# Kernel optimization log

Hardware: AMD Instinct MI355X
Metric: run time of the kernel (lower is better)

## Reference

```python
import jax, jax.numpy as jnp
import numpy as np

CONV_NUM = 8
CONV_SIZE = 96
HIDDEN = 768  # = CONV_NUM * CONV_SIZE
MAX_LEN = 128


def get_entity(x, s, e):
    # x: [B, L, H]; mean of x[i, s[i]:max(e[i], s[i]+1)] per sample (ragged gather+mean)
    e = jnp.maximum(e, s + 1)
    pos = jnp.arange(x.shape[1])  # [L]
    mask = (pos[None, :] >= s[:, None]) & (pos[None, :] < e[:, None])  # [B, L]
    m = mask.astype(x.dtype)
    return jnp.einsum('blh,bl->bh', x, m) / jnp.sum(m, axis=1, keepdims=True)


def feature_abstract(head_ent, tail_ent, x, fc_W, fc_b):
    # head_ent/tail_ent: [B, HIDDEN] -> per-sample conv filters; x: [B, HIDDEN]
    B = x.shape[0]
    wh = head_ent.reshape(B * CONV_NUM, 1, 1, CONV_SIZE)
    wt = tail_ent.reshape(B * CONV_NUM, 1, 1, CONV_SIZE)
    lhs = x.reshape(1, B, 1, HIDDEN)  # NCHW, groups=B -> per-sample correlation
    h = jax.nn.relu(jax.lax.conv_general_dilated(lhs, wh, (1, 1), 'VALID', feature_group_count=B))
    t = jax.nn.relu(jax.lax.conv_general_dilated(lhs, wt, (1, 1), 'VALID', feature_group_count=B))
    # h,t: [1, B*CONV_NUM, 1, T] with T = HIDDEN - CONV_SIZE + 1
    ht = jnp.concatenate([h, t], axis=3).reshape(B * CONV_NUM, -1)  # [B*cn, 2T]
    ht = ht.reshape(B * CONV_NUM, -1, 2).mean(axis=-1)  # AvgPool1d(k=2, s=2) -> [B*cn, T]
    flat = ht.reshape(B, -1)  # [B, cn*T] (dropout is identity in eval)
    return flat @ fc_W.T + fc_b  # [B, HIDDEN]


def setup_inputs() -> dict:
    key = jax.random.key(0)
    ks = jax.random.split(key, 16)
    Bs, Bq, L, H = 400, 1200, MAX_LEN, HIDDEN

    def spans(k1, k2, B):
        s = jax.random.randint(k1, (B,), 0, 100)
        e = jnp.minimum(s + jax.random.randint(k2, (B,), 1, 20), L)
        return s.astype(jnp.int64), e.astype(jnp.int64)

    s_eh, s_eh_end = spans(ks[0], ks[1], Bs)
    s_et, s_et_end = spans(ks[2], ks[3], Bs)
    q_eh, q_eh_end = spans(ks[4], ks[5], Bq)
    q_et, q_et_end = spans(ks[6], ks[7], Bq)
    fc_in = (H - CONV_SIZE + 1) * CONV_NUM  # 5384
    return {
        'all_support': jax.random.normal(ks[8], (Bs, L, H), jnp.float32),
        'support_emb': jax.random.normal(ks[9], (Bs, H), jnp.float32),
        'all_query': jax.random.normal(ks[10], (Bq, L, H), jnp.float32),
        'query_emb': jax.random.normal(ks[11], (Bq, H), jnp.float32),
        'fc_W': jax.random.normal(ks[12], (H, fc_in), jnp.float32) / np.sqrt(fc_in),
        'fc_b': jnp.zeros((H,), jnp.float32),
        's_eh': s_eh, 's_eh_end': s_eh_end, 's_et': s_et, 's_et_end': s_et_end,
        'q_eh': q_eh, 'q_eh_end': q_eh_end, 'q_et': q_et, 'q_et_end': q_et_end,
        'N': 10, 'K': 5, 'total_Q': 150,
    }


def reference(all_support, support_emb, all_query, query_emb, fc_W, fc_b,
              s_eh, s_eh_end, s_et, s_et_end, q_eh, q_eh_end, q_et, q_et_end,
              N, K, total_Q):
    sh = get_entity(all_support, s_eh, s_eh_end)
    st = get_entity(all_support, s_et, s_et_end)
    qh = get_entity(all_query, q_eh, q_eh_end)
    qt = get_entity(all_query, q_et, q_et_end)

    sup = feature_abstract(sh, st, support_emb, fc_W, fc_b).reshape(-1, N, K, HIDDEN)
    qry = feature_abstract(qh, qt, query_emb, fc_W, fc_b).reshape(-1, total_Q, HIDDEN)

    proto = sup.mean(axis=2)  # [Be, N, H]
    # -||proto - query||^2 over feature dim -> [Be, total_Q, N]
    diff = proto[:, None, :, :] - qry[:, :, None, :]
    logits = -jnp.sum(diff * diff, axis=-1)
    minn = logits.min(axis=-1)
    logits = jnp.concatenate([logits, minn[..., None] - 1.0], axis=2)  # [Be, total_Q, N+1]
    pred = jnp.argmax(logits.reshape(-1, N + 1), axis=1)
    return logits, pred
```

## Files before the change

kernel.cpp:

```cpp
#include <hip/hip_runtime.h>

#define H        768
#define LMAX     128
#define CONV_NUM 8
#define CONV_SIZE 96
#define T_CONV   673
#define FC_IN    5384
#define KP       5408
#define KSTEPS   (KP / 32)
#define N_WAY    10
#define K_SHOT   5
#define TOTAL_Q  150
#define SPLITK   8
#define BS       400
#define BQ       1200
#define MTOT     1600
#define NPROTO   80
#define MA       1280

using s16x8 = __attribute__((ext_vector_type(8))) short;
using f32x4 = __attribute__((ext_vector_type(4))) float;
typedef unsigned short u16;

__device__ __forceinline__ u16 f2bf(float x) {
    unsigned u = __float_as_uint(x);
    u += 0x7FFFu + ((u >> 16) & 1u);
    return (u16)(u >> 16);
}
__device__ __forceinline__ float bf2f(u16 b) { return __uint_as_float(((unsigned)b) << 16); }

__device__ __forceinline__ void gl16(const u16* g, u16* l) {
    __builtin_amdgcn_global_load_lds(
        (const __attribute__((address_space(1))) unsigned int*)g,
        (__attribute__((address_space(3))) unsigned int*)l, 16, 0, 0);
}

#define HTS 678
#define XCS 784
__global__ __launch_bounds__(256, 4) void pre_kernel(
    const float* __restrict__ all_support, const float* __restrict__ all_query,
    const float* __restrict__ support_emb, const float* __restrict__ query_emb,
    const float* __restrict__ fc_W,
    const int* __restrict__ s_eh, const int* __restrict__ s_eh_end,
    const int* __restrict__ s_et, const int* __restrict__ s_et_end,
    const int* __restrict__ q_eh, const int* __restrict__ q_eh_end,
    const int* __restrict__ q_et, const int* __restrict__ q_et_end,
    u16* __restrict__ flatS, u16* __restrict__ A_bf,
    u16* __restrict__ Wh)
{
    int bid = blockIdx.x;
    int tid = threadIdx.x;

    if (bid >= MTOT) {
        int r = bid - MTOT;
        for (int j = tid; j < KP; j += 256) {
            float v = (j < FC_IN) ? fc_W[(size_t)r * FC_IN + j] : 0.f;
            Wh[(size_t)r * KP + j] = f2bf(v);
        }
        return;
    }

    __shared__ u16 htb[16 * HTS];
    __shared__ u16 filt_h[16 * 96];
    __shared__ u16 filt_l[16 * 96];
    __shared__ u16 xcs[8][XCS];
    float* xs = (float*)htb;

    int b = bid;
    const float* src;
    int sh, eh, st, et;
    if (b < BS) {
        src = all_support + (size_t)b * LMAX * H;
        sh = s_eh[b]; eh = s_eh_end[b]; st = s_et[b]; et = s_et_end[b];
    } else {
        int m = b - BS;
        src = all_query + (size_t)m * LMAX * H;
        sh = q_eh[m]; eh = q_eh_end[m]; st = q_et[m]; et = q_et_end[m];
    }
    if (eh < sh + 1) eh = sh + 1;
    if (et < st + 1) et = st + 1;

    {
        float a0 = 0.f, a1 = 0.f, a2 = 0.f;
        for (int r = sh; r < eh; ++r) {
            const float* row = src + (size_t)r * H;
            a0 += row[tid]; a1 += row[tid + 256]; a2 += row[tid + 512];
        }
        float rc = 1.0f / (float)(eh - sh);
        float m0 = a0 * rc, m1 = a1 * rc, m2 = a2 * rc;
        u16 h0 = f2bf(m0), h1 = f2bf(m1), h2 = f2bf(m2);
        filt_h[tid] = h0;       filt_l[tid] = f2bf(m0 - bf2f(h0));
        filt_h[tid + 256] = h1; filt_l[tid + 256] = f2bf(m1 - bf2f(h1));
        filt_h[tid + 512] = h2; filt_l[tid + 512] = f2bf(m2 - bf2f(h2));
        a0 = a1 = a2 = 0.f;
        for (int r = st; r < et; ++r) {
            const float* row = src + (size_t)r * H;
            a0 += row[tid]; a1 += row[tid + 256]; a2 += row[tid + 512];
        }
        rc = 1.0f / (float)(et - st);
        m0 = a0 * rc; m1 = a1 * rc; m2 = a2 * rc;
        h0 = f2bf(m0); h1 = f2bf(m1); h2 = f2bf(m2);
        filt_h[tid + 768] = h0;  filt_l[tid + 768] = f2bf(m0 - bf2f(h0));
        filt_h[tid + 1024] = h1; filt_l[tid + 1024] = f2bf(m1 - bf2f(h1));
        filt_h[tid + 1280] = h2; filt_l[tid + 1280] = f2bf(m2 - bf2f(h2));
    }
    const float* xsrc = (b < BS) ? (support_emb + (size_t)b * H)
                                 : (query_emb + (size_t)(b - BS) * H);
    if (tid < 192)
        *(float4*)&xs[tid * 4] = *(const float4*)&xsrc[tid * 4];
    if (tid >= 192 && tid < 200) {
        int o = 768 + (tid - 192) * 4;
        xs[o] = 0.f; xs[o + 1] = 0.f; xs[o + 2] = 0.f; xs[o + 3] = 0.f;
    }
    __syncthreads();

    #pragma unroll 1
    for (int c = 0; c < 8; ++c)
        for (int i = tid; i < XCS; i += 256)
            xcs[c][i] = f2bf(xs[i + c]);
    __syncthreads();

    {
        int lane = tid & 63, wv = tid >> 6;
        int n = lane & 15, g = lane >> 4;
        int afo = n * 96 + g * 8;
        s16x8 fh0 = *(const s16x8*)&filt_h[afo];
        s16x8 fh1 = *(const s16x8*)&filt_h[afo + 32];
        s16x8 fh2 = *(const s16x8*)&filt_h[afo + 64];
        s16x8 fl0 = *(const s16x8*)&filt_l[afo];
        s16x8 fl1 = *(const s16x8*)&filt_l[afo + 32];
        s16x8 fl2 = *(const s16x8*)&filt_l[afo + 64];
        const u16* xrow = &xcs[n & 7][g * 8 + (n & 8)];
        #pragma unroll 1
        for (int nt = wv; nt < 43; nt += 4) {
            const u16* xp = xrow + nt * 16;
            s16x8 x0 = *(const s16x8*)(xp);
            s16x8 x1 = *(const s16x8*)(xp + 32);
            s16x8 x2 = *(const s16x8*)(xp + 64);
            f32x4 a = (f32x4){0.f, 0.f, 0.f, 0.f};
            a = __builtin_amdgcn_mfma_f32_16x16x32_bf16(fh0, x0, a, 0, 0, 0);
            a = __builtin_amdgcn_mfma_f32_16x16x32_bf16(fl0, x0, a, 0, 0, 0);
            a = __builtin_amdgcn_mfma_f32_16x16x32_bf16(fh1, x1, a, 0, 0, 0);
            a = __builtin_amdgcn_mfma_f32_16x16x32_bf16(fl1, x1, a, 0, 0, 0);
            a = __builtin_amdgcn_mfma_f32_16x16x32_bf16(fh2, x2, a, 0, 0, 0);
            a = __builtin_amdgcn_mfma_f32_16x16x32_bf16(fl2, x2, a, 0, 0, 0);
            int pcol = nt * 16 + n;
            if (pcol < T_CONV) {
                #pragma unroll
                for (int r = 0; r < 4; ++r)
                    htb[(g * 4 + r) * HTS + pcol] = f2bf(fmaxf(a[r], 0.f));
            }
        }
    }
    __syncthreads();

    u16* oh = (b < BS) ? (flatS + (size_t)b * KP)
                       : (A_bf + (size_t)(NPROTO + b - BS) * KP);
    for (int f = 0; f < CONV_NUM; ++f) {
        for (int j = tid; j < T_CONV; j += 256) {
            int i0 = 2 * j, i1 = 2 * j + 1;
            float v0 = bf2f((i0 < T_CONV) ? htb[f * HTS + i0]
                                          : htb[(8 + f) * HTS + (i0 - T_CONV)]);
            float v1 = bf2f((i1 < T_CONV) ? htb[f * HTS + i1]
                                          : htb[(8 + f) * HTS + (i1 - T_CONV)]);
            oh[f * T_CONV + j] = f2bf(0.5f * (v0 + v1));
        }
    }
    for (int j = FC_IN + tid; j < KP; j += 256) oh[j] = 0;
}

__global__ __launch_bounds__(256) void avg_kernel(
    const u16* __restrict__ flatS, u16* __restrict__ A_bf)
{
    int i = blockIdx.x;
    size_t base = (size_t)i * K_SHOT * KP;
    for (int t = threadIdx.x; t < KP / 8; t += 256) {
        int j = t * 8;
        float s[8] = {0.f, 0.f, 0.f, 0.f, 0.f, 0.f, 0.f, 0.f};
        #pragma unroll
        for (int k = 0; k < K_SHOT; ++k) {
            s16x8 vh = *(const s16x8*)(flatS + base + (size_t)k * KP + j);
            #pragma unroll
            for (int u = 0; u < 8; ++u)
                s[u] += bf2f((u16)vh[u]);
        }
        s16x8 oh;
        #pragma unroll
        for (int u = 0; u < 8; ++u)
            oh[u] = (short)f2bf(s[u] * (1.0f / K_SHOT));
        *(s16x8*)(A_bf + (size_t)i * KP + j) = oh;
    }
}

#define ASEG 8192
#define BSEG 4096
#define BUFU (ASEG + BSEG)

#define STAGE(ks, buf) do {                                     \
    int kb_ = (ks) * 32;                                        \
    u16* L_ = &lds[buf][0];                                     \
    gl16(Ah_g + aoff0 + kb_, L_ + cA0 * 8);                     \
    gl16(Ah_g + aoff1 + kb_, L_ + cA1 * 8);                     \
    gl16(Ah_g + aoff2 + kb_, L_ + cA2 * 8);                     \
    gl16(Ah_g + aoff3 + kb_, L_ + cA3 * 8);                     \
    gl16(Bh_g + boff0 + kb_, L_ + ASEG + cB0 * 8);              \
    gl16(Bh_g + boff1 + kb_, L_ + ASEG + cB1 * 8);              \
} while (0)

__global__ __launch_bounds__(256, 2) void gemm_mfma(
    const u16* __restrict__ Ah_g, const u16* __restrict__ Bh_g,
    u16* __restrict__ partsB)
{
    __shared__ u16 lds[2][BUFU];

    int tid = threadIdx.x;
    int wg = (blockIdx.x & 7) * 30 + (blockIdx.x >> 3);
    int sk = wg / 30;
    int rem = wg % 30;
    int n0 = (rem / 5) * 128;
    int m0 = (rem % 5) * 256;

    int ks0 = (KSTEPS * sk) / SPLITK;
    int nk = (KSTEPS * (sk + 1)) / SPLITK - ks0;

    int cA0 = tid, cA1 = tid + 256, cA2 = tid + 512, cA3 = tid + 768;
    int cB0 = tid, cB1 = tid + 256;
    size_t aoff0 = (size_t)(m0 + (cA0 >> 6) * 16 + (cA0 & 15)) * KP + ((cA0 >> 4) & 3) * 8;
    size_t aoff1 = (size_t)(m0 + (cA1 >> 6) * 16 + (cA1 & 15)) * KP + ((cA1 >> 4) & 3) * 8;
    size_t aoff2 = (size_t)(m0 + (cA2 >> 6) * 16 + (cA2 & 15)) * KP + ((cA2 >> 4) & 3) * 8;
    size_t aoff3 = (size_t)(m0 + (cA3 >> 6) * 16 + (cA3 & 15)) * KP + ((cA3 >> 4) & 3) * 8;
    size_t boff0 = (size_t)(n0 + (cB0 >> 6) * 16 + (cB0 & 15)) * KP + ((cB0 >> 4) & 3) * 8;
    size_t boff1 = (size_t)(n0 + (cB1 >> 6) * 16 + (cB1 & 15)) * KP + ((cB1 >> 4) & 3) * 8;

    int w = tid >> 6, lane = tid & 63;
    int lfr = ((lane >> 4) * 16 + (lane & 15)) * 8;

    f32x4 acc[4][8];
    #pragma unroll
    for (int i = 0; i < 4; ++i)
        #pragma unroll
        for (int j = 0; j < 8; ++j) acc[i][j] = (f32x4){0.f, 0.f, 0.f, 0.f};

    STAGE(ks0, 0);
    STAGE(ks0 + 1, 1);

    int cur = 0;
    for (int k = 0; k < nk; ++k) {
        if (k + 1 < nk) asm volatile("s_waitcnt vmcnt(6)" ::: "memory");
        else            asm volatile("s_waitcnt vmcnt(0)" ::: "memory");
        __builtin_amdgcn_s_barrier();

        const u16* L = &lds[cur][0];
        s16x8 ah[4], bh[8];
        #pragma unroll
        for (int f = 0; f < 4; ++f)
            ah[f] = *(const s16x8*)(L + (w * 4 + f) * 512 + lfr);
        #pragma unroll
        for (int j = 0; j < 8; ++j)
            bh[j] = *(const s16x8*)(L + ASEG + j * 512 + lfr);
        asm volatile("s_waitcnt lgkmcnt(0)" ::: "memory");
        __builtin_amdgcn_s_barrier();

        if (k + 2 < nk) STAGE(ks0 + k + 2, cur);

        #pragma unroll
        for (int i = 0; i < 4; ++i)
            #pragma unroll
            for (int j = 0; j < 8; ++j)
                acc[i][j] = __builtin_amdgcn_mfma_f32_16x16x32_bf16(ah[i], bh[j], acc[i][j], 0, 0, 0);
        cur ^= 1;
    }

    int rbase = m0 + w * 64 + (lane >> 4) * 4;
    int cbase = n0 + (lane & 15);
    #pragma unroll
    for (int i = 0; i < 4; ++i) {
        int row0 = rbase + i * 16;
        #pragma unroll
        for (int j = 0; j < 8; ++j) {
            int col = cbase + j * 16;
            u16* dst = partsB + ((size_t)sk * MA + row0) * H + col;
            #pragma unroll
            for (int r = 0; r < 4; ++r)
                dst[(size_t)r * H] = f2bf(acc[i][j][r]);
        }
    }
}

__global__ __launch_bounds__(256) void protofin_kernel(
    const u16* __restrict__ partsB, float* __restrict__ proto)
{
    int i = blockIdx.x;
    int tid = threadIdx.x;
    #pragma unroll
    for (int q = 0; q < 3; ++q) {
        int d = tid + q * 256;
        float s = 0.f;
        #pragma unroll
        for (int sp = 0; sp < SPLITK; ++sp)
            s += bf2f(partsB[((size_t)sp * MA + i) * H + d]);
        proto[(size_t)i * H + d] = s;
    }
}

__global__ __launch_bounds__(256) void dist_kernel(
    const u16* __restrict__ partsB, const float* __restrict__ proto,
    float* __restrict__ outp)
{
    int bid = blockIdx.x;
    int e = bid / TOTAL_Q;
    int tid = threadIdx.x;
    int m = NPROTO + bid;

    float qv[3];
    #pragma unroll
    for (int q = 0; q < 3; ++q) {
        int d = tid + q * 256;
        float s = 0.f;
        #pragma unroll
        for (int sp = 0; sp < SPLITK; ++sp)
            s += bf2f(partsB[((size_t)sp * MA + m) * H + d]);
        qv[q] = s;
    }

    __shared__ float red[N_WAY][4];
    __shared__ float lvals[N_WAY];
    int wave = tid >> 6, lane = tid & 63;
    for (int n = 0; n < N_WAY; ++n) {
        const float* pr = proto + (size_t)(e * N_WAY + n) * H;
        float p = 0.f;
        #pragma unroll
        for (int q = 0; q < 3; ++q) {
            int d = tid + q * 256;
            float df = pr[d] - qv[q];
            p = fmaf(df, df, p);
        }
        #pragma unroll
        for (int off = 32; off > 0; off >>= 1)
            p += __shfl_down(p, off);
        if (lane == 0) red[n][wave] = p;
    }
    __syncthreads();
    if (tid < N_WAY) {
        float v = red[tid][0] + red[tid][1] + red[tid][2] + red[tid][3];
        lvals[tid] = -v;
        outp[(size_t)bid * (N_WAY + 1) + tid] = -v;
    }
    __syncthreads();
    if (tid == 0) {
        float mn = lvals[0];
        #pragma unroll
        for (int n = 1; n < N_WAY; ++n) mn = fminf(mn, lvals[n]);
        float last = mn - 1.0f;
        outp[(size_t)bid * (N_WAY + 1) + N_WAY] = last;
        float best = lvals[0];
        int bi = 0;
        for (int n = 1; n < N_WAY; ++n)
            if (lvals[n] > best) { best = lvals[n]; bi = n; }
        if (last > best) bi = N_WAY;
        outp[(size_t)BQ * (N_WAY + 1) + bid] = (float)bi;
    }
}

extern "C" void kernel_launch(void* const* d_in, const int* in_sizes, int n_in,
                              void* d_out, int out_size, void* d_ws, size_t ws_size,
                              hipStream_t stream)
{
    const float* all_support = (const float*)d_in[0];
    const float* support_emb = (const float*)d_in[1];
    const float* all_query   = (const float*)d_in[2];
    const float* query_emb   = (const float*)d_in[3];
    const float* fc_W        = (const float*)d_in[4];
    const int* s_eh     = (const int*)d_in[6];
    const int* s_eh_end = (const int*)d_in[7];
    const int* s_et     = (const int*)d_in[8];
    const int* s_et_end = (const int*)d_in[9];
    const int* q_eh     = (const int*)d_in[10];
    const int* q_eh_end = (const int*)d_in[11];
    const int* q_et     = (const int*)d_in[12];
    const int* q_et_end = (const int*)d_in[13];

    u16* partsB  = (u16*)d_ws;
    float* proto = (float*)(partsB + (size_t)SPLITK * MA * H);
    u16* Wh      = (u16*)(proto + (size_t)NPROTO * H);
    u16* A_bf    = Wh + (size_t)H * KP;
    u16* flatS   = A_bf + (size_t)MA * KP;

    pre_kernel<<<MTOT + H, 256, 0, stream>>>(
        all_support, all_query, support_emb, query_emb, fc_W,
        s_eh, s_eh_end, s_et, s_et_end, q_eh, q_eh_end, q_et, q_et_end,
        flatS, A_bf, Wh);

    avg_kernel<<<NPROTO, 256, 0, stream>>>(flatS, A_bf);

    gemm_mfma<<<240, 256, 0, stream>>>(A_bf, Wh, partsB);

    protofin_kernel<<<NPROTO, 256, 0, stream>>>(partsB, proto);

    dist_kernel<<<BQ, 256, 0, stream>>>(partsB, proto, (float*)d_out);
}
```

Before: 74.75 us.

## Vectorize weight conversion, unroll span gather, fuse shifted-copy build, vectorize dist loads

The fc_W to bf16 conversion now uses float4 loads and ushort4 stores. The entity span-mean loops are unrolled by two with dual accumulators to expose more loads in flight. The per-channel shifted bf16 copies of x are written straight from registers, dropping the fp32 staging buffer and one barrier. The distance kernel reads partial sums and prototypes as 4-wide vectors, which leaves a quarter of the threads idle in exchange for fewer, wider memory transactions.

```diff
diff --git a/kernel.cpp b/kernel.cpp
--- a/kernel.cpp
+++ b/kernel.cpp
@@ -53,9 +53,18 @@
 
     if (bid >= MTOT) {
         int r = bid - MTOT;
-        for (int j = tid; j < KP; j += 256) {
-            float v = (j < FC_IN) ? fc_W[(size_t)r * FC_IN + j] : 0.f;
-            Wh[(size_t)r * KP + j] = f2bf(v);
+        const float* wr = fc_W + (size_t)r * FC_IN;
+        u16* whr = Wh + (size_t)r * KP;
+        for (int j4 = tid; j4 < KP / 4; j4 += 256) {
+            int j = j4 * 4;
+            ushort4 o;
+            if (j4 < FC_IN / 4) {
+                float4 v = *(const float4*)(wr + j);
+                o.x = f2bf(v.x); o.y = f2bf(v.y); o.z = f2bf(v.z); o.w = f2bf(v.w);
+            } else {
+                o.x = 0; o.y = 0; o.z = 0; o.w = 0;
+            }
+            *(ushort4*)(whr + j) = o;
         }
         return;
     }
@@ -64,7 +73,6 @@
     __shared__ u16 filt_h[16 * 96];
     __shared__ u16 filt_l[16 * 96];
     __shared__ u16 xcs[8][XCS];
-    float* xs = (float*)htb;
 
     int b = bid;
     const float* src;
@@ -81,43 +89,64 @@
     if (et < st + 1) et = st + 1;
 
     {
-        float a0 = 0.f, a1 = 0.f, a2 = 0.f;
-        for (int r = sh; r < eh; ++r) {
-            const float* row = src + (size_t)r * H;
-            a0 += row[tid]; a1 += row[tid + 256]; a2 += row[tid + 512];
+        float a0 = 0.f, a1 = 0.f, a2 = 0.f, b0 = 0.f, b1 = 0.f, b2 = 0.f;
+        int r = sh;
+        for (; r + 2 <= eh; r += 2) {
+            const float* p0 = src + (size_t)r * H;
+            const float* p1 = p0 + H;
+            a0 += p0[tid]; a1 += p0[tid + 256]; a2 += p0[tid + 512];
+            b0 += p1[tid]; b1 += p1[tid + 256]; b2 += p1[tid + 512];
+        }
+        if (r < eh) {
+            const float* p0 = src + (size_t)r * H;
+            a0 += p0[tid]; a1 += p0[tid + 256]; a2 += p0[tid + 512];
         }
         float rc = 1.0f / (float)(eh - sh);
-        float m0 = a0 * rc, m1 = a1 * rc, m2 = a2 * rc;
+        float m0 = (a0 + b0) * rc, m1 = (a1 + b1) * rc, m2 = (a2 + b2) * rc;
         u16 h0 = f2bf(m0), h1 = f2bf(m1), h2 = f2bf(m2);
         filt_h[tid] = h0;       filt_l[tid] = f2bf(m0 - bf2f(h0));
         filt_h[tid + 256] = h1; filt_l[tid + 256] = f2bf(m1 - bf2f(h1));
         filt_h[tid + 512] = h2; filt_l[tid + 512] = f2bf(m2 - bf2f(h2));
-        a0 = a1 = a2 = 0.f;
-        for (int r = st; r < et; ++r) {
-            const float* row = src + (size_t)r * H;
-            a0 += row[tid]; a1 += row[tid + 256]; a2 += row[tid + 512];
+        a0 = a1 = a2 = b0 = b1 = b2 = 0.f;
+        r = st;
+        for (; r + 2 <= et; r += 2) {
+            const float* p0 = src + (size_t)r * H;
+            const float* p1 = p0 + H;
+            a0 += p0[tid]; a1 += p0[tid + 256]; a2 += p0[tid + 512];
+            b0 += p1[tid]; b1 += p1[tid + 256]; b2 += p1[tid + 512];
+        }
+        if (r < et) {
+            const float* p0 = src + (size_t)r * H;
+            a0 += p0[tid]; a1 += p0[tid + 256]; a2 += p0[tid + 512];
         }
         rc = 1.0f / (float)(et - st);
-        m0 = a0 * rc; m1 = a1 * rc; m2 = a2 * rc;
+        m0 = (a0 + b0) * rc; m1 = (a1 + b1) * rc; m2 = (a2 + b2) * rc;
         h0 = f2bf(m0); h1 = f2bf(m1); h2 = f2bf(m2);
         filt_h[tid + 768] = h0;  filt_l[tid + 768] = f2bf(m0 - bf2f(h0));
         filt_h[tid + 1024] = h1; filt_l[tid + 1024] = f2bf(m1 - bf2f(h1));
         filt_h[tid + 1280] = h2; filt_l[tid + 1280] = f2bf(m2 - bf2f(h2));
     }
-    const float* xsrc = (b < BS) ? (support_emb + (size_t)b * H)
-                                 : (query_emb + (size_t)(b - BS) * H);
-    if (tid < 192)
-        *(float4*)&xs[tid * 4] = *(const float4*)&xsrc[tid * 4];
-    if (tid >= 192 && tid < 200) {
-        int o = 768 + (tid - 192) * 4;
-        xs[o] = 0.f; xs[o + 1] = 0.f; xs[o + 2] = 0.f; xs[o + 3] = 0.f;
-    }
-    __syncthreads();
-
-    #pragma unroll 1
-    for (int c = 0; c < 8; ++c)
-        for (int i = tid; i < XCS; i += 256)
-            xcs[c][i] = f2bf(xs[i + c]);
+
+    {
+        if (tid < 192) {
+            int row = tid / 24, idx = tid % 24;
+            int j = 768 - row + idx;
+            if (j < XCS) xcs[row][j] = 0;
+        }
+        const float* xsrc = (b < BS) ? (support_emb + (size_t)b * H)
+                                     : (query_emb + (size_t)(b - BS) * H);
+        if (tid < 192) {
+            float4 v = *(const float4*)(xsrc + tid * 4);
+            u16 h[4] = {f2bf(v.x), f2bf(v.y), f2bf(v.z), f2bf(v.w)};
+            #pragma unroll
+            for (int u = 0; u < 4; ++u) {
+                int i = tid * 4 + u;
+                #pragma unroll
+                for (int c = 0; c < 8; ++c)
+                    if (i >= c) xcs[c][i - c] = h[u];
+            }
+        }
+    }
     __syncthreads();
 
     {
@@ -311,29 +340,30 @@
     int e = bid / TOTAL_Q;
     int tid = threadIdx.x;
     int m = NPROTO + bid;
-
-    float qv[3];
-    #pragma unroll
-    for (int q = 0; q < 3; ++q) {
-        int d = tid + q * 256;
-        float s = 0.f;
-        #pragma unroll
-        for (int sp = 0; sp < SPLITK; ++sp)
-            s += bf2f(partsB[((size_t)sp * MA + m) * H + d]);
-        qv[q] = s;
+    int d0 = tid * 4;
+
+    float qv0 = 0.f, qv1 = 0.f, qv2 = 0.f, qv3 = 0.f;
+    if (tid < 192) {
+        #pragma unroll
+        for (int sp = 0; sp < SPLITK; ++sp) {
+            ushort4 v = *(const ushort4*)(partsB + ((size_t)sp * MA + m) * H + d0);
+            qv0 += bf2f(v.x); qv1 += bf2f(v.y); qv2 += bf2f(v.z); qv3 += bf2f(v.w);
+        }
     }
 
     __shared__ float red[N_WAY][4];
     __shared__ float lvals[N_WAY];
     int wave = tid >> 6, lane = tid & 63;
     for (int n = 0; n < N_WAY; ++n) {
-        const float* pr = proto + (size_t)(e * N_WAY + n) * H;
         float p = 0.f;
-        #pragma unroll
-        for (int q = 0; q < 3; ++q) {
-            int d = tid + q * 256;
-            float df = pr[d] - qv[q];
-            p = fmaf(df, df, p);
+        if (tid < 192) {
+            const float* pr = proto + (size_t)(e * N_WAY + n) * H + d0;
+            float4 pv = *(const float4*)pr;
+            float df0 = pv.x - qv0, df1 = pv.y - qv1, df2 = pv.z - qv2, df3 = pv.w - qv3;
+            p = df0 * df0;
+            p = fmaf(df1, df1, p);
+            p = fmaf(df2, df2, p);
+            p = fmaf(df3, df3, p);
         }
         #pragma unroll
         for (int off = 32; off > 0; off >>= 1)
```

After: 69.77 us. 1.07x faster.
